# Kernel optimization log

Measured on AMD Instinct MI355X. Metric: run time of the kernel, lower is better.

## Reference

```python
import jax, jax.numpy as jnp
import numpy as np

B, T, RSS, L, FEAT, H = 256, 256, 12, 256, 8, 128
DIST_EPS = 1e-8
LN_EPS = 1e-5

def _lin(x, W, b):
    return x @ W.T + b

def setup_inputs() -> dict:
    key = jax.random.key(0)
    ks = jax.random.split(key, 20)
    w = lambda k, shape: jax.random.normal(k, shape, jnp.float32) * 0.1
    z = lambda *s: jnp.zeros(s, jnp.float32)
    # LED table: xyz positions in a room, frequency index in 1..12 (matches rss channels)
    pos = jax.random.uniform(ks[0], (L, 3), jnp.float32, 0.0, 5.0)
    freq = jax.random.randint(ks[1], (L,), 1, RSS + 1).astype(jnp.float32)
    return dict(
        rss_seq=jax.random.uniform(ks[2], (B, T, RSS), jnp.float32),
        global_led_pos_freq=jnp.concatenate([pos, freq[:, None]], axis=1),
        enc_W1=w(ks[3], (32, 4)), enc_b1=z(32), enc_W2=w(ks[4], (FEAT, 32)), enc_b2=z(FEAT),
        q_W1=w(ks[5], (64, 4)), q_b1=z(64), q_W2=w(ks[6], (64, 64)), q_b2=z(64),
        k_W1=w(ks[7], (64, FEAT + 3)), k_b1=z(64), k_W2=w(ks[8], (64, 64)), k_b2=z(64),
        Wih0=w(ks[9], (4 * H, RSS * (1 + FEAT))), Whh0=w(ks[10], (4 * H, H)), bih0=z(4 * H), bhh0=z(4 * H),
        Wih1=w(ks[11], (4 * H, H)), Whh1=w(ks[12], (4 * H, H)), bih1=z(4 * H), bhh1=z(4 * H),
        ln_g=jnp.ones((H,), jnp.float32), ln_b=z(H),
        fc_W1=w(ks[13], (H // 2, H)), fc_b1=z(H // 2), fc_W2=w(ks[14], (3, H // 2)), fc_b2=z(3),
    )

def _lstm_cell(x, h, c, Wih, Whh, bih, bhh):
    g = x @ Wih.T + bih + h @ Whh.T + bhh  # [B, 4H], pytorch gate order i,f,g,o
    i, f, gg, o = jnp.split(g, 4, axis=-1)
    c = jax.nn.sigmoid(f) * c + jax.nn.sigmoid(i) * jnp.tanh(gg)
    h = jax.nn.sigmoid(o) * jnp.tanh(c)
    return h, c

def _forward(rss_seq, global_led_pos_freq, enc_W1, enc_b1, enc_W2, enc_b2,
             q_W1, q_b1, q_W2, q_b2, k_W1, k_b1, k_W2, k_b2,
             Wih0, Whh0, bih0, bhh0, Wih1, Whh1, bih1, bhh1,
             ln_g, ln_b, fc_W1, fc_b1, fc_W2, fc_b2):
    batch, t_len, rss_dim = rss_seq.shape
    led_pos = global_led_pos_freq[:, :3]   # [L,3]
    led_freq = global_led_pos_freq[:, 3]   # [L]
    rss_freqs = jnp.arange(1, rss_dim + 1, dtype=rss_seq.dtype)
    freq_mask = rss_freqs[:, None] == led_freq[None, :]  # [RSS, L] bool
    # global LED features are a buffer computed under no_grad in torch
    led_feat = jax.lax.stop_gradient(
        jax.nn.relu(_lin(jax.nn.relu(_lin(global_led_pos_freq, enc_W1, enc_b1)), enc_W2, enc_b2)))  # [L,FEAT]
    keys = _lin(jax.nn.relu(_lin(jnp.concatenate([led_feat, led_pos], axis=1), k_W1, k_b1)), k_W2, k_b2)  # [L,64]
    neg = jnp.finfo(rss_seq.dtype).min

    def step(carry, rss_t):
        prev_pos, h0, c0, h1, c1 = carry  # prev_pos [B,3]
        q_in = jnp.concatenate(
            [rss_t[..., None], jnp.broadcast_to(prev_pos[:, None, :], (batch, rss_dim, 3))], axis=-1)  # [B,RSS,4]
        q = _lin(jax.nn.relu(_lin(q_in, q_W1, q_b1)), q_W2, q_b2)  # [B,RSS,64]
        scores = jnp.einsum('bqd,ld->bql', q, keys)  # [B,RSS,L]
        dist_sq = jnp.sum((prev_pos[:, None, :] - led_pos[None, :, :]) ** 2, axis=-1)  # [B,L]
        scores = scores + (-0.5 * jnp.log(dist_sq + DIST_EPS))[:, None, :]
        scores = jnp.where(freq_mask[None], scores, neg)
        attn = jax.nn.softmax(scores, axis=-1)
        agg = jnp.einsum('bql,lf->bqf', attn, led_feat)  # [B,RSS,FEAT]
        x = jnp.concatenate([rss_t[..., None], agg], axis=-1).reshape(batch, -1)  # [B, RSS*(1+FEAT)]
        h0n, c0n = _lstm_cell(x, h0, c0, Wih0, Whh0, bih0, bhh0)
        h1n, c1n = _lstm_cell(h0n, h1, c1, Wih1, Whh1, bih1, bhh1)
        y = h1n
        mu = jnp.mean(y, axis=-1, keepdims=True)
        var = jnp.var(y, axis=-1, keepdims=True)
        y = (y - mu) / jnp.sqrt(var + LN_EPS) * ln_g + ln_b
        pred = _lin(jax.nn.relu(_lin(y, fc_W1, fc_b1)), fc_W2, fc_b2)  # [B,3]
        return (pred, h0n, c0n, h1n, c1n), pred

    prev0 = jnp.broadcast_to(jnp.mean(led_pos, axis=0, keepdims=True), (batch, 3))
    hz = jnp.zeros((batch, Whh0.shape[1]), rss_seq.dtype)
    _, outs = jax.lax.scan(step, (prev0, hz, hz, hz, hz), jnp.swapaxes(rss_seq, 0, 1))
    return jnp.swapaxes(outs, 0, 1)  # [B,T,3]

def reference(rss_seq, global_led_pos_freq, enc_W1, enc_b1, enc_W2, enc_b2,
              q_W1, q_b1, q_W2, q_b2, k_W1, k_b1, k_W2, k_b2,
              Wih0, Whh0, bih0, bhh0, Wih1, Whh1, bih1, bhh1,
              ln_g, ln_b, fc_W1, fc_b1, fc_W2, fc_b2):
    return _forward(rss_seq, global_led_pos_freq, enc_W1, enc_b1, enc_W2, enc_b2,
                    q_W1, q_b1, q_W2, q_b2, k_W1, k_b1, k_W2, k_b2,
                    Wih0, Whh0, bih0, bhh0, Wih1, Whh1, bih1, bhh1,
                    ln_g, ln_b, fc_W1, fc_b1, fc_W2, fc_b2)
```

## Files before the change

kernel.cpp:

```cpp
#include <hip/hip_runtime.h>
#include <hip/hip_fp16.h>
#include <math.h>

#define B_ 256
#define T_ 256
#define RSS_ 12
#define L_ 256
#define FEAT_ 8
#define H_ 128

constexpr int OFF_PW0  = 0;
constexpr int OFF_PW1  = OFF_PW0 + 63488;
constexpr int OFF_W1L  = OFF_PW1 + 32768;
constexpr int OFF_B0   = OFF_W1L + 32768;
constexpr int OFF_B1   = OFF_B0 + 512;
constexpr int OFF_QW1T = OFF_B1 + 512;
constexpr int OFF_FC1  = OFF_QW1T + 256;
constexpr int OFF_K2T4 = OFF_FC1 + 8192;
constexpr int OFF_KB   = OFF_K2T4 + 16384;
constexpr int OFF_LF   = OFF_KB + 256;
constexpr int OFF_LPX  = OFF_LF + 2048;
constexpr int OFF_LPY  = OFF_LPX + 256;
constexpr int OFF_LPZ  = OFF_LPY + 256;
constexpr int OFF_MEAN = OFF_LPZ + 256;
constexpr int OFF_PREV0= OFF_MEAN + 8;
constexpr int OFF_INT  = OFF_PREV0 + 4;

__device__ __forceinline__ unsigned packh2(float a, float b) {
  const unsigned short lo = __half_as_ushort(__float2half(a));
  const unsigned short hi = __half_as_ushort(__float2half(b));
  return (unsigned)lo | ((unsigned)hi << 16);
}
__device__ __forceinline__ __half2 u2h2(unsigned u){ union { unsigned u; __half2 h; } c; c.u = u; return c.h; }
__device__ __forceinline__ float sigf(float x){ return 1.f/(1.f+expf(-x)); }

#if __has_builtin(__builtin_amdgcn_fdot2)
typedef _Float16 h2v __attribute__((ext_vector_type(2)));
__device__ __forceinline__ float d2(unsigned w, unsigned z, float acc) {
  union { unsigned u; h2v h; } cw, cz; cw.u = w; cz.u = z;
  return __builtin_amdgcn_fdot2(cw.h, cz.h, acc, false);
}
#else
__device__ __forceinline__ float d2(unsigned w, unsigned z, float acc) {
  const __half2 hw = u2h2(w), hz = u2h2(z);
  acc = fmaf(__low2float(hw),  __low2float(hz),  acc);
  return fmaf(__high2float(hw), __high2float(hz), acc);
}
#endif

constexpr int SZ_PW0 = 63488, SZ_PW1 = 32768, SZ_W1L = 32768, SZ_B = 512, SZ_Q = 256, SZ_FC = 8192;
constexpr int TOT_T = SZ_PW0 + SZ_PW1 + SZ_W1L + SZ_B + SZ_B + SZ_Q + SZ_FC;

__global__ void k_prep(const float* __restrict__ Wih0, const float* __restrict__ Whh0,
                       const float* __restrict__ bih0, const float* __restrict__ bhh0,
                       const float* __restrict__ Wih1, const float* __restrict__ Whh1,
                       const float* __restrict__ bih1, const float* __restrict__ bhh1,
                       const float* __restrict__ qW1,  const float* __restrict__ fcW1,
                       float* __restrict__ ws) {
  unsigned* wsu = (unsigned*)ws;
  for (int t = blockIdx.x*blockDim.x + threadIdx.x; t < TOT_T; t += gridDim.x*blockDim.x) {
    int u = t;
    if (u < SZ_PW0) {
      const int k = u & 3, j = (u >> 2) & 511, q = u >> 11;
      const int p = 4*q + k;
      float lo, hi;
      if (p < 60) {
        const int r = p / 5, e0 = 2*(p % 5), e1 = e0 + 1;
        lo = Wih0[j*108 + r*9 + e0];
        hi = (e1 <= 8) ? Wih0[j*108 + r*9 + e1] : 0.f;
      } else {
        const int i0 = 2*(p - 60);
        lo = Whh0[j*128 + i0]; hi = Whh0[j*128 + i0 + 1];
      }
      wsu[OFF_PW0 + u] = packh2(lo, hi); continue;
    } u -= SZ_PW0;
    if (u < SZ_PW1) {
      const int k = u & 3, j = (u >> 2) & 511, q = u >> 11;
      const int i0 = 2*(4*q + k);
      wsu[OFF_PW1 + u] = packh2(Wih1[j*128 + i0], Wih1[j*128 + i0 + 1]); continue;
    } u -= SZ_PW1;
    if (u < SZ_W1L) {
      const int k = u & 3, j = (u >> 2) & 511, q = u >> 11;
      const int i0 = 2*(4*q + k);
      wsu[OFF_W1L + u] = packh2(Whh1[j*128 + i0], Whh1[j*128 + i0 + 1]); continue;
    } u -= SZ_W1L;
    if (u < SZ_B) { ws[OFF_B0+u] = bih0[u]+bhh0[u]; continue; } u -= SZ_B;
    if (u < SZ_B) { ws[OFF_B1+u] = bih1[u]+bhh1[u]; continue; } u -= SZ_B;
    if (u < SZ_Q) { const int c=u>>6, j=u&63; ws[OFF_QW1T+u] = qW1[j*4+c]; continue; } u -= SZ_Q;
    { const int c = u >> 8, rem = u & 255, j = rem >> 2, k = rem & 3;
      ws[OFF_FC1 + u] = fcW1[j*128 + (c<<2) + k]; }
  }
}

__global__ __launch_bounds__(256) void k_led(const float* __restrict__ gplf,
    const float* __restrict__ encW1, const float* __restrict__ encb1,
    const float* __restrict__ encW2, const float* __restrict__ encb2,
    const float* __restrict__ kW1, const float* __restrict__ kb1,
    const float* __restrict__ kW2, const float* __restrict__ kb2,
    const float* __restrict__ qW2, const float* __restrict__ qb2,
    float* __restrict__ ws) {
  __shared__ float sLF[L_][FEAT_];
  __shared__ float sP[L_][3];
  __shared__ int   sR[L_];
  const int l = threadIdx.x;
  const float p0=gplf[l*4+0], p1=gplf[l*4+1], p2=gplf[l*4+2], fr=gplf[l*4+3];

  float e1[32];
  for (int j=0;j<32;++j) {
    float v = encb1[j] + encW1[j*4+0]*p0 + encW1[j*4+1]*p1 + encW1[j*4+2]*p2 + encW1[j*4+3]*fr;
    e1[j] = fmaxf(v,0.f);
  }
  float lf[8];
  for (int f=0;f<8;++f) {
    float v = encb2[f];
    for (int j=0;j<32;++j) v += encW2[f*32+j]*e1[j];
    lf[f] = fmaxf(v,0.f);
  }
  float kin[11] = {lf[0],lf[1],lf[2],lf[3],lf[4],lf[5],lf[6],lf[7],p0,p1,p2};
  float hh[64];
  for (int j=0;j<64;++j) {
    float v = kb1[j];
    for (int c=0;c<11;++c) v += kW1[j*11+c]*kin[c];
    hh[j]=fmaxf(v,0.f);
  }
  float kk[64];
  for (int d=0;d<64;++d) {
    float v = kb2[d];
    for (int j=0;j<64;++j) v += kW2[d*64+j]*hh[j];
    kk[d]=v;
  }
  float kbv=0.f;
  for (int d=0;d<64;++d) kbv += qb2[d]*kk[d];
  ws[OFF_KB+l]=kbv;
  for (int e=0;e<64;++e) {
    float acc=0.f;
    for (int d=0;d<64;++d) acc += qW2[d*64+e]*kk[d];
    ws[OFF_K2T4 + (e>>2)*1024 + l*4 + (e&3)] = acc;
  }
  for (int f=0;f<8;++f){ ws[OFF_LF+l*8+f]=lf[f]; sLF[l][f]=lf[f]; }
  ws[OFF_LPX+l]=p0; ws[OFF_LPY+l]=p1; ws[OFF_LPZ+l]=p2;
  sP[l][0]=p0; sP[l][1]=p1; sP[l][2]=p2;
  const int r = (int)fr - 1;
  sR[l]=r;
  int* iws = (int*)(ws + OFF_INT);
  iws[l] = r;
  __syncthreads();
  if (l==0) {
    int* cntp = iws + 256;
    int* idxp = cntp + 16;
    int c[12]; for (int r2=0;r2<12;++r2) c[r2]=0;
    for (int i=0;i<L_;++i){ int r2=sR[i]; idxp[r2*256 + c[r2]] = i; c[r2]++; }
    for (int r2=0;r2<12;++r2) cntp[r2]=c[r2];
    float mx=0.f,my=0.f,mz=0.f;
    for (int i=0;i<L_;++i){mx+=sP[i][0];my+=sP[i][1];mz+=sP[i][2];}
    ws[OFF_PREV0+0]=mx/(float)L_; ws[OFF_PREV0+1]=my/(float)L_; ws[OFF_PREV0+2]=mz/(float)L_;
    for (int f=0;f<8;++f){ float s=0.f; for (int i=0;i<L_;++i) s+=sLF[i][f]; ws[OFF_MEAN+f]=s/(float)L_; }
  }
}

__global__ __launch_bounds__(512,1) void k_main(const float* __restrict__ rss,
    const float* __restrict__ qb1, const float* __restrict__ lng, const float* __restrict__ lnb,
    const float* __restrict__ fcb1, const float* __restrict__ fcW2, const float* __restrict__ fcb2,
    const float* __restrict__ ws, float* __restrict__ out) {
  const int b = blockIdx.x, tid = threadIdx.x;
  const int lane = tid & 63, wave = tid >> 6;
  const int j = tid;

  __shared__ uint4 sW1L[8192];
  __shared__ unsigned sLFh[1024];
  __shared__ float sLPx[256], sLPy[256], sLPz[256];
  __shared__ float sKB[256];
  __shared__ float sQ[256], sqb1v[64];
  __shared__ float sLNG[128], sLNB[128];
  __shared__ float sfcb1[64], sfcW2v[192], sfcb2v[4];
  __shared__ float sMEANv[8];
  __shared__ __align__(16) unsigned sz0h[124];
  __shared__ __align__(16) unsigned sz1h[128];
  __shared__ float sc0[128], sc1[128];
  __shared__ __align__(16) float sa[12][68];
  __shared__ float ssv[256];
  __shared__ float sg[512];
  __shared__ __align__(16) float syv[128];
  __shared__ float sprev[4];
  __shared__ int   sledR[256], scnt[16];
  __shared__ unsigned short sidx16[12*256];

  const uint4* PW0 = (const uint4*)((const unsigned*)ws + OFF_PW0);
  const uint4* PW1 = (const uint4*)((const unsigned*)ws + OFF_PW1);
#define LW0(Q) uint4 w0_##Q = PW0[Q*512 + j];
#define LW1(Q) uint4 w1_##Q = PW1[Q*512 + j];
  LW0(0) LW0(1) LW0(2) LW0(3) LW0(4) LW0(5) LW0(6) LW0(7) LW0(8) LW0(9)
  LW0(10) LW0(11) LW0(12) LW0(13) LW0(14) LW0(15) LW0(16) LW0(17) LW0(18) LW0(19)
  LW0(20) LW0(21) LW0(22) LW0(23) LW0(24) LW0(25) LW0(26) LW0(27) LW0(28) LW0(29) LW0(30)
  LW1(0) LW1(1) LW1(2) LW1(3) LW1(4) LW1(5) LW1(6) LW1(7)
  LW1(8) LW1(9) LW1(10) LW1(11) LW1(12) LW1(13) LW1(14) LW1(15)
  float biasA = ws[OFF_B0 + j];
  float biasB = ws[OFF_B1 + j];
#define PIN4(V) asm volatile("" : "+v"(V.x), "+v"(V.y), "+v"(V.z), "+v"(V.w));
  PIN4(w0_0) PIN4(w0_1) PIN4(w0_2) PIN4(w0_3) PIN4(w0_4) PIN4(w0_5) PIN4(w0_6) PIN4(w0_7)
  PIN4(w0_8) PIN4(w0_9) PIN4(w0_10) PIN4(w0_11) PIN4(w0_12) PIN4(w0_13) PIN4(w0_14) PIN4(w0_15)
  PIN4(w0_16) PIN4(w0_17) PIN4(w0_18) PIN4(w0_19) PIN4(w0_20) PIN4(w0_21) PIN4(w0_22) PIN4(w0_23)
  PIN4(w0_24) PIN4(w0_25) PIN4(w0_26) PIN4(w0_27) PIN4(w0_28) PIN4(w0_29) PIN4(w0_30)
  PIN4(w1_0) PIN4(w1_1) PIN4(w1_2) PIN4(w1_3) PIN4(w1_4) PIN4(w1_5) PIN4(w1_6) PIN4(w1_7)
  PIN4(w1_8) PIN4(w1_9) PIN4(w1_10) PIN4(w1_11) PIN4(w1_12) PIN4(w1_13) PIN4(w1_14) PIN4(w1_15)
  asm volatile("" : "+v"(biasA), "+v"(biasB));

  {
    const uint4* W1Lg = (const uint4*)((const unsigned*)ws + OFF_W1L);
    for (int u = tid; u < 8192; u += 512) sW1L[u] = W1Lg[u];
    for (int u = tid; u < 1024; u += 512) sLFh[u] = packh2(ws[OFF_LF+2*u], ws[OFF_LF+2*u+1]);
  }
  if (tid < 256) { sLPx[tid]=ws[OFF_LPX+tid]; sLPy[tid]=ws[OFF_LPY+tid]; sLPz[tid]=ws[OFF_LPZ+tid];
                   sKB[tid]=ws[OFF_KB+tid]; sQ[tid]=ws[OFF_QW1T+tid]; }
  if (tid < 64) { sqb1v[tid]=qb1[tid]; sfcb1[tid]=fcb1[tid]; }
  if (tid < 128){ sLNG[tid]=lng[tid]; sLNB[tid]=lnb[tid]; sc0[tid]=0.f; sc1[tid]=0.f; sz1h[tid]=0u; }
  if (tid < 192) sfcW2v[tid]=fcW2[tid];
  if (tid < 3)  { sfcb2v[tid]=fcb2[tid]; sprev[tid]=ws[OFF_PREV0+tid]; }
  if (tid < 8)   sMEANv[tid]=ws[OFF_MEAN+tid];
  if (tid < 64)  sz0h[60+tid]=0u;
  {
    const int* iws = (const int*)(ws + OFF_INT);
    if (tid < 256) sledR[tid]=iws[tid];
    if (tid < 12)  scnt[tid]=iws[256+tid];
    for (int u = tid; u < 12*256; u += 512) sidx16[u] = (unsigned short)iws[272+u];
  }
  __syncthreads();

  const float* rb = rss + (size_t)b*T_*12;
  float x0 = rb[wave];
  float x1 = (wave < 4) ? rb[wave+8] : 0.f;

  const float4* K2g = (const float4*)(ws + OFF_K2T4);
  const float4* F1g = (const float4*)(ws + OFF_FC1);
  const uint4*  z0u4 = (const uint4*)sz0h;
  const uint4*  z1u4 = (const uint4*)sz1h;

  for (int t = 0; t < T_; ++t) {
    float xn0 = 0.f, xn1 = 0.f;
    if (t+1 < T_) {
      xn0 = rb[(t+1)*12 + wave];
      if (wave < 4) xn1 = rb[(t+1)*12 + wave+8];
    }
    const float px = sprev[0], py = sprev[1], pz = sprev[2];

    {
      float v = sqb1v[lane] + x0*sQ[lane] + px*sQ[64+lane] + py*sQ[128+lane] + pz*sQ[192+lane];
      sa[wave][lane] = fmaxf(v, 0.f);
      if (wave < 4) {
        float v2 = sqb1v[lane] + x1*sQ[lane] + px*sQ[64+lane] + py*sQ[128+lane] + pz*sQ[192+lane];
        sa[wave+8][lane] = fmaxf(v2, 0.f);
      }
    }
    __syncthreads();

    if (tid < 256) {
      const int l = tid, r = sledR[l];
      float a0 = sKB[l], a1 = 0.f;
      const float4* ar4 = (const float4*)&sa[r][0];
      #pragma unroll 1
      for (int cc = 0; cc < 4; ++cc) {
        const float4 wA = K2g[(cc*4+0)*256 + l];
        const float4 wB = K2g[(cc*4+1)*256 + l];
        const float4 wC = K2g[(cc*4+2)*256 + l];
        const float4 wD = K2g[(cc*4+3)*256 + l];
        const float4 aA = ar4[cc*4+0], aB = ar4[cc*4+1], aC = ar4[cc*4+2], aD = ar4[cc*4+3];
        a0=fmaf(aA.x,wA.x,a0); a1=fmaf(aA.y,wA.y,a1); a0=fmaf(aA.z,wA.z,a0); a1=fmaf(aA.w,wA.w,a1);
        a0=fmaf(aB.x,wB.x,a0); a1=fmaf(aB.y,wB.y,a1); a0=fmaf(aB.z,wB.z,a0); a1=fmaf(aB.w,wB.w,a1);
        a0=fmaf(aC.x,wC.x,a0); a1=fmaf(aC.y,wC.y,a1); a0=fmaf(aC.z,wC.z,a0); a1=fmaf(aC.w,wC.w,a1);
        a0=fmaf(aD.x,wD.x,a0); a1=fmaf(aD.y,wD.y,a1); a0=fmaf(aD.z,wD.z,a0); a1=fmaf(aD.w,wD.w,a1);
      }
      const float dx = px-sLPx[tid], dy = py-sLPy[tid], dz = pz-sLPz[tid];
      ssv[tid] = a0 + a1 - 0.5f*logf(dx*dx+dy*dy+dz*dz + 1e-8f);
    }
    __syncthreads();

    for (int rr = 0; rr < 2; ++rr) {
      if (rr == 1 && wave >= 4) break;
      const int r = wave + rr*8;
      const int cnt = scnt[r];
      float vmax = -3.402823466e38f;
      for (int c = lane; c < cnt; c += 64) vmax = fmaxf(vmax, ssv[sidx16[r*256+c]]);
      #pragma unroll
      for (int o = 32; o > 0; o >>= 1) vmax = fmaxf(vmax, __shfl_xor(vmax, o));
      float ps=0.f, p0=0.f,p1=0.f,p2=0.f,p3=0.f,p4=0.f,p5=0.f,p6=0.f,p7=0.f;
      for (int c = lane; c < cnt; c += 64) {
        const int li = sidx16[r*256+c];
        const float p = expf(ssv[li]-vmax);
        ps += p;
        const unsigned* lf = sLFh + li*4;
        const __half2 A=u2h2(lf[0]), Bq=u2h2(lf[1]), C=u2h2(lf[2]), D=u2h2(lf[3]);
        p0 += p*__low2float(A); p1 += p*__high2float(A);
        p2 += p*__low2float(Bq); p3 += p*__high2float(Bq);
        p4 += p*__low2float(C); p5 += p*__high2float(C);
        p6 += p*__low2float(D); p7 += p*__high2float(D);
      }
      #pragma unroll
      for (int o = 32; o > 0; o >>= 1) {
        ps += __shfl_xor(ps,o);
        p0 += __shfl_xor(p0,o); p1 += __shfl_xor(p1,o);
        p2 += __shfl_xor(p2,o); p3 += __shfl_xor(p3,o);
        p4 += __shfl_xor(p4,o); p5 += __shfl_xor(p5,o);
        p6 += __shfl_xor(p6,o); p7 += __shfl_xor(p7,o);
      }
      if (lane == 0) {
        const float xv = rr ? x1 : x0;
        float a0v,a1v,a2v,a3v,a4v,a5v,a6v,a7v;
        if (cnt > 0) {
          const float inv = 1.f/ps;
          a0v=p0*inv; a1v=p1*inv; a2v=p2*inv; a3v=p3*inv;
          a4v=p4*inv; a5v=p5*inv; a6v=p6*inv; a7v=p7*inv;
        } else {
          a0v=sMEANv[0]; a1v=sMEANv[1]; a2v=sMEANv[2]; a3v=sMEANv[3];
          a4v=sMEANv[4]; a5v=sMEANv[5]; a6v=sMEANv[6]; a7v=sMEANv[7];
        }
        sz0h[r*5+0] = packh2(xv,  a0v);
        sz0h[r*5+1] = packh2(a1v, a2v);
        sz0h[r*5+2] = packh2(a3v, a4v);
        sz0h[r*5+3] = packh2(a5v, a6v);
        sz0h[r*5+4] = packh2(a7v, 0.f);
      }
    }
    __syncthreads();

    {
      float g0 = biasA, g1 = 0.f, g2 = 0.f, g3 = 0.f;
#define D0(Q) { const uint4 Z = z0u4[Q]; \
      g0 = d2(w0_##Q.x, Z.x, g0); g1 = d2(w0_##Q.y, Z.y, g1); \
      g2 = d2(w0_##Q.z, Z.z, g2); g3 = d2(w0_##Q.w, Z.w, g3); }
      D0(0) D0(1) D0(2) D0(3) D0(4) D0(5) D0(6) D0(7) D0(8) D0(9)
      D0(10) D0(11) D0(12) D0(13) D0(14) D0(15) D0(16) D0(17) D0(18) D0(19)
      D0(20) D0(21) D0(22) D0(23) D0(24) D0(25) D0(26) D0(27) D0(28) D0(29) D0(30)
      sg[j] = (g0+g1)+(g2+g3);
    }
    __syncthreads();

    if (tid < 64) {
      const int v = tid;
      const float iA=sigf(sg[2*v]),     iB=sigf(sg[2*v+1]);
      const float fA=sigf(sg[128+2*v]), fB=sigf(sg[128+2*v+1]);
      const float gA=tanhf(sg[256+2*v]),gB=tanhf(sg[256+2*v+1]);
      const float oA=sigf(sg[384+2*v]), oB=sigf(sg[384+2*v+1]);
      const float cA = fA*sc0[2*v]   + iA*gA;
      const float cB = fB*sc0[2*v+1] + iB*gB;
      sc0[2*v] = cA; sc0[2*v+1] = cB;
      const float hA = oA*tanhf(cA), hB = oB*tanhf(cB);
      const unsigned hp = packh2(hA, hB);
      sz0h[60+v] = hp; sz1h[v] = hp;
    }
    __syncthreads();

    {
      float g0 = biasB, g1 = 0.f, g2 = 0.f, g3 = 0.f;
#define E1(Q) { const uint4 Z = z1u4[Q]; \
      g0 = d2(w1_##Q.x, Z.x, g0); g1 = d2(w1_##Q.y, Z.y, g1); \
      g2 = d2(w1_##Q.z, Z.z, g2); g3 = d2(w1_##Q.w, Z.w, g3); }
      E1(0) E1(1) E1(2) E1(3) E1(4) E1(5) E1(6) E1(7)
      E1(8) E1(9) E1(10) E1(11) E1(12) E1(13) E1(14) E1(15)
      #pragma unroll 4
      for (int q = 0; q < 16; ++q) {
        const uint4 W = sW1L[q*512 + j];
        const uint4 Z = z1u4[16+q];
        g0 = d2(W.x, Z.x, g0); g1 = d2(W.y, Z.y, g1);
        g2 = d2(W.z, Z.z, g2); g3 = d2(W.w, Z.w, g3);
      }
      sg[j] = (g0+g1)+(g2+g3);
    }
    __syncthreads();

    if (tid < 64) {
      const int v = tid;
      const float iA=sigf(sg[2*v]),     iB=sigf(sg[2*v+1]);
      const float fA=sigf(sg[128+2*v]), fB=sigf(sg[128+2*v+1]);
      const float gA=tanhf(sg[256+2*v]),gB=tanhf(sg[256+2*v+1]);
      const float oA=sigf(sg[384+2*v]), oB=sigf(sg[384+2*v+1]);
      const float cA = fA*sc1[2*v]   + iA*gA;
      const float cB = fB*sc1[2*v+1] + iB*gB;
      sc1[2*v] = cA; sc1[2*v+1] = cB;
      const float hA = oA*tanhf(cA), hB = oB*tanhf(cB);
      sz1h[64+v] = packh2(hA, hB);
      float s = hA + hB, qs = hA*hA + hB*hB;
      #pragma unroll
      for (int o = 32; o > 0; o >>= 1) { s += __shfl_xor(s,o); qs += __shfl_xor(qs,o); }
      const float mu = s*(1.f/128.f);
      const float rs = 1.f/sqrtf(qs*(1.f/128.f) - mu*mu + 1e-5f);
      const float yA = (hA-mu)*rs*sLNG[2*v] + sLNB[2*v];
      const float yB = (hB-mu)*rs*sLNG[2*v+1] + sLNB[2*v+1];
      syv[2*v] = yA; syv[2*v+1] = yB;
      float acc = sfcb1[v], acc2 = 0.f;
      const float4* sy4 = (const float4*)syv;
      #pragma unroll 1
      for (int cc = 0; cc < 8; ++cc) {
        const float4 wA = F1g[(cc*4+0)*64 + v];
        const float4 wB = F1g[(cc*4+1)*64 + v];
        const float4 wC = F1g[(cc*4+2)*64 + v];
        const float4 wD = F1g[(cc*4+3)*64 + v];
        const float4 zA = sy4[cc*4+0], zB = sy4[cc*4+1], zC = sy4[cc*4+2], zD = sy4[cc*4+3];
        acc=fmaf(wA.x,zA.x,acc); acc2=fmaf(wA.y,zA.y,acc2); acc=fmaf(wA.z,zA.z,acc); acc2=fmaf(wA.w,zA.w,acc2);
        acc=fmaf(wB.x,zB.x,acc); acc2=fmaf(wB.y,zB.y,acc2); acc=fmaf(wB.z,zB.z,acc); acc2=fmaf(wB.w,zB.w,acc2);
        acc=fmaf(wC.x,zC.x,acc); acc2=fmaf(wC.y,zC.y,acc2); acc=fmaf(wC.z,zC.z,acc); acc2=fmaf(wC.w,zC.w,acc2);
        acc=fmaf(wD.x,zD.x,acc); acc2=fmaf(wD.y,zD.y,acc2); acc=fmaf(wD.z,zD.z,acc); acc2=fmaf(wD.w,zD.w,acc2);
      }
      const float f1 = fmaxf(acc+acc2, 0.f);
      float a0 = sfcW2v[v]*f1, a1 = sfcW2v[64+v]*f1, a2 = sfcW2v[128+v]*f1;
      #pragma unroll
      for (int o = 32; o > 0; o >>= 1) {
        a0 += __shfl_xor(a0,o); a1 += __shfl_xor(a1,o); a2 += __shfl_xor(a2,o);
      }
      if (v < 3) {
        const float r = (v==0 ? a0 : (v==1 ? a1 : a2)) + sfcb2v[v];
        out[((size_t)b*T_+t)*3+v] = r;
        sprev[v] = r;
      }
    }
    __syncthreads();

    x0 = xn0; x1 = xn1;
  }
}

extern "C" void kernel_launch(void* const* d_in, const int* in_sizes, int n_in,
                              void* d_out, int out_size, void* d_ws, size_t ws_size,
                              hipStream_t stream) {
  const float* rss   = (const float*)d_in[0];
  const float* gplf  = (const float*)d_in[1];
  const float* encW1 = (const float*)d_in[2];
  const float* encb1 = (const float*)d_in[3];
  const float* encW2 = (const float*)d_in[4];
  const float* encb2 = (const float*)d_in[5];
  const float* qW1   = (const float*)d_in[6];
  const float* qb1   = (const float*)d_in[7];
  const float* qW2   = (const float*)d_in[8];
  const float* qb2   = (const float*)d_in[9];
  const float* kW1   = (const float*)d_in[10];
  const float* kb1   = (const float*)d_in[11];
  const float* kW2   = (const float*)d_in[12];
  const float* kb2   = (const float*)d_in[13];
  const float* Wih0  = (const float*)d_in[14];
  const float* Whh0  = (const float*)d_in[15];
  const float* bih0  = (const float*)d_in[16];
  const float* bhh0  = (const float*)d_in[17];
  const float* Wih1  = (const float*)d_in[18];
  const float* Whh1  = (const float*)d_in[19];
  const float* bih1  = (const float*)d_in[20];
  const float* bhh1  = (const float*)d_in[21];
  const float* lng   = (const float*)d_in[22];
  const float* lnb   = (const float*)d_in[23];
  const float* fcW1  = (const float*)d_in[24];
  const float* fcb1  = (const float*)d_in[25];
  const float* fcW2  = (const float*)d_in[26];
  const float* fcb2  = (const float*)d_in[27];
  float* ws   = (float*)d_ws;
  float* outp = (float*)d_out;

  hipLaunchKernelGGL(k_prep, dim3(256), dim3(256), 0, stream,
                     Wih0,Whh0,bih0,bhh0,Wih1,Whh1,bih1,bhh1,qW1,fcW1,ws);
  hipLaunchKernelGGL(k_led, dim3(1), dim3(256), 0, stream,
                     gplf,encW1,encb1,encW2,encb2,kW1,kb1,kW2,kb2,qW2,qb2,ws);
  hipLaunchKernelGGL(k_main, dim3(B_), dim3(512), 0, stream,
                     rss,qb1,lng,lnb,fcb1,fcW2,fcb2,ws,outp);
}
```

Baseline: 2.746 ms.

## Double block to 1024 threads, split LSTM gate dot products across halves

Launches k_main with 1024 threads per block. Each LSTM gate row's reduction over the packed input/hidden vector is split between two thread halves, and the partial sums are combined through a two-slot shared buffer before the activations. The LED key MLP is spread over four threads per LED with a shuffle reduction, and each frequency channel gets its own wave. The aim is to shorten the serial per-timestep critical path and halve the register-pinned weights per thread, at the cost of more synchronising threads and an extra shared-memory add per gate.

```diff
diff --git a/kernel.cpp b/kernel.cpp
--- a/kernel.cpp
+++ b/kernel.cpp
@@ -158,13 +158,13 @@
   }
 }
 
-__global__ __launch_bounds__(512,1) void k_main(const float* __restrict__ rss,
+__global__ __launch_bounds__(1024) void k_main(const float* __restrict__ rss,
     const float* __restrict__ qb1, const float* __restrict__ lng, const float* __restrict__ lnb,
     const float* __restrict__ fcb1, const float* __restrict__ fcW2, const float* __restrict__ fcb2,
     const float* __restrict__ ws, float* __restrict__ out) {
   const int b = blockIdx.x, tid = threadIdx.x;
   const int lane = tid & 63, wave = tid >> 6;
-  const int j = tid;
+  const int j = tid & 511, h = tid >> 9;
 
   __shared__ uint4 sW1L[8192];
   __shared__ unsigned sLFh[1024];
@@ -179,7 +179,7 @@
   __shared__ float sc0[128], sc1[128];
   __shared__ __align__(16) float sa[12][68];
   __shared__ float ssv[256];
-  __shared__ float sg[512];
+  __shared__ float sgp[2][512];
   __shared__ __align__(16) float syv[128];
   __shared__ float sprev[4];
   __shared__ int   sledR[256], scnt[16];
@@ -187,48 +187,45 @@
 
   const uint4* PW0 = (const uint4*)((const unsigned*)ws + OFF_PW0);
   const uint4* PW1 = (const uint4*)((const unsigned*)ws + OFF_PW1);
-#define LW0(Q) uint4 w0_##Q = PW0[Q*512 + j];
-#define LW1(Q) uint4 w1_##Q = PW1[Q*512 + j];
-  LW0(0) LW0(1) LW0(2) LW0(3) LW0(4) LW0(5) LW0(6) LW0(7) LW0(8) LW0(9)
-  LW0(10) LW0(11) LW0(12) LW0(13) LW0(14) LW0(15) LW0(16) LW0(17) LW0(18) LW0(19)
-  LW0(20) LW0(21) LW0(22) LW0(23) LW0(24) LW0(25) LW0(26) LW0(27) LW0(28) LW0(29) LW0(30)
+  const int zb0 = h * 15;
+#define LW0(Q) uint4 w0_##Q = PW0[(zb0+Q)*512 + j];
+  LW0(0) LW0(1) LW0(2) LW0(3) LW0(4) LW0(5) LW0(6) LW0(7)
+  LW0(8) LW0(9) LW0(10) LW0(11) LW0(12) LW0(13) LW0(14)
+  uint4 w0x = h ? PW0[30*512 + j] : make_uint4(0,0,0,0);
+#define LW1(Q) uint4 w1_##Q = PW1[(h*8+Q)*512 + j];
   LW1(0) LW1(1) LW1(2) LW1(3) LW1(4) LW1(5) LW1(6) LW1(7)
-  LW1(8) LW1(9) LW1(10) LW1(11) LW1(12) LW1(13) LW1(14) LW1(15)
-  float biasA = ws[OFF_B0 + j];
-  float biasB = ws[OFF_B1 + j];
+  float biasA = h ? 0.f : ws[OFF_B0 + j];
+  float biasB = h ? 0.f : ws[OFF_B1 + j];
 #define PIN4(V) asm volatile("" : "+v"(V.x), "+v"(V.y), "+v"(V.z), "+v"(V.w));
   PIN4(w0_0) PIN4(w0_1) PIN4(w0_2) PIN4(w0_3) PIN4(w0_4) PIN4(w0_5) PIN4(w0_6) PIN4(w0_7)
-  PIN4(w0_8) PIN4(w0_9) PIN4(w0_10) PIN4(w0_11) PIN4(w0_12) PIN4(w0_13) PIN4(w0_14) PIN4(w0_15)
-  PIN4(w0_16) PIN4(w0_17) PIN4(w0_18) PIN4(w0_19) PIN4(w0_20) PIN4(w0_21) PIN4(w0_22) PIN4(w0_23)
-  PIN4(w0_24) PIN4(w0_25) PIN4(w0_26) PIN4(w0_27) PIN4(w0_28) PIN4(w0_29) PIN4(w0_30)
+  PIN4(w0_8) PIN4(w0_9) PIN4(w0_10) PIN4(w0_11) PIN4(w0_12) PIN4(w0_13) PIN4(w0_14) PIN4(w0x)
   PIN4(w1_0) PIN4(w1_1) PIN4(w1_2) PIN4(w1_3) PIN4(w1_4) PIN4(w1_5) PIN4(w1_6) PIN4(w1_7)
-  PIN4(w1_8) PIN4(w1_9) PIN4(w1_10) PIN4(w1_11) PIN4(w1_12) PIN4(w1_13) PIN4(w1_14) PIN4(w1_15)
   asm volatile("" : "+v"(biasA), "+v"(biasB));
 
   {
     const uint4* W1Lg = (const uint4*)((const unsigned*)ws + OFF_W1L);
-    for (int u = tid; u < 8192; u += 512) sW1L[u] = W1Lg[u];
-    for (int u = tid; u < 1024; u += 512) sLFh[u] = packh2(ws[OFF_LF+2*u], ws[OFF_LF+2*u+1]);
+    for (int u = tid; u < 8192; u += 1024) sW1L[u] = W1Lg[u];
+    for (int u = tid; u < 1024; u += 1024) sLFh[u] = packh2(ws[OFF_LF+2*u], ws[OFF_LF+2*u+1]);
   }
   if (tid < 256) { sLPx[tid]=ws[OFF_LPX+tid]; sLPy[tid]=ws[OFF_LPY+tid]; sLPz[tid]=ws[OFF_LPZ+tid];
                    sKB[tid]=ws[OFF_KB+tid]; sQ[tid]=ws[OFF_QW1T+tid]; }
-  if (tid < 64) { sqb1v[tid]=qb1[tid]; sfcb1[tid]=fcb1[tid]; }
-  if (tid < 128){ sLNG[tid]=lng[tid]; sLNB[tid]=lnb[tid]; sc0[tid]=0.f; sc1[tid]=0.f; sz1h[tid]=0u; }
-  if (tid < 192) sfcW2v[tid]=fcW2[tid];
-  if (tid < 3)  { sfcb2v[tid]=fcb2[tid]; sprev[tid]=ws[OFF_PREV0+tid]; }
-  if (tid < 8)   sMEANv[tid]=ws[OFF_MEAN+tid];
-  if (tid < 64)  sz0h[60+tid]=0u;
+  else if (tid >= 256 && tid < 320) { sqb1v[tid-256]=qb1[tid-256]; sfcb1[tid-256]=fcb1[tid-256]; }
+  else if (tid >= 320 && tid < 448) { sLNG[tid-320]=lng[tid-320]; sLNB[tid-320]=lnb[tid-320];
+                                      sc0[tid-320]=0.f; sc1[tid-320]=0.f; sz1h[tid-320]=0u; }
+  else if (tid >= 448 && tid < 640) sfcW2v[tid-448]=fcW2[tid-448];
+  else if (tid >= 640 && tid < 643) { sfcb2v[tid-640]=fcb2[tid-640]; sprev[tid-640]=ws[OFF_PREV0+tid-640]; }
+  else if (tid >= 648 && tid < 656) sMEANv[tid-648]=ws[OFF_MEAN+tid-648];
+  else if (tid >= 656 && tid < 720) sz0h[60+(tid-656)]=0u;
   {
     const int* iws = (const int*)(ws + OFF_INT);
-    if (tid < 256) sledR[tid]=iws[tid];
-    if (tid < 12)  scnt[tid]=iws[256+tid];
-    for (int u = tid; u < 12*256; u += 512) sidx16[u] = (unsigned short)iws[272+u];
+    if (tid >= 720 && tid < 976) sledR[tid-720]=iws[tid-720];
+    if (tid >= 976 && tid < 988) scnt[tid-976]=iws[256+(tid-976)];
+    for (int u = tid; u < 12*256; u += 1024) sidx16[u] = (unsigned short)iws[272+u];
   }
   __syncthreads();
 
   const float* rb = rss + (size_t)b*T_*12;
-  float x0 = rb[wave];
-  float x1 = (wave < 4) ? rb[wave+8] : 0.f;
+  float x0 = (wave < 12) ? rb[wave] : 0.f;
 
   const float4* K2g = (const float4*)(ws + OFF_K2T4);
   const float4* F1g = (const float4*)(ws + OFF_FC1);
@@ -236,48 +233,41 @@
   const uint4*  z1u4 = (const uint4*)sz1h;
 
   for (int t = 0; t < T_; ++t) {
-    float xn0 = 0.f, xn1 = 0.f;
-    if (t+1 < T_) {
-      xn0 = rb[(t+1)*12 + wave];
-      if (wave < 4) xn1 = rb[(t+1)*12 + wave+8];
-    }
+    float xn0 = 0.f;
+    if (t+1 < T_ && wave < 12) xn0 = rb[(t+1)*12 + wave];
     const float px = sprev[0], py = sprev[1], pz = sprev[2];
 
-    {
+    if (tid < 768) {
       float v = sqb1v[lane] + x0*sQ[lane] + px*sQ[64+lane] + py*sQ[128+lane] + pz*sQ[192+lane];
       sa[wave][lane] = fmaxf(v, 0.f);
-      if (wave < 4) {
-        float v2 = sqb1v[lane] + x1*sQ[lane] + px*sQ[64+lane] + py*sQ[128+lane] + pz*sQ[192+lane];
-        sa[wave+8][lane] = fmaxf(v2, 0.f);
-      }
-    }
-    __syncthreads();
-
-    if (tid < 256) {
-      const int l = tid, r = sledR[l];
-      float a0 = sKB[l], a1 = 0.f;
+    }
+    __syncthreads();
+
+    {
+      const int l = tid >> 2, k = tid & 3;
+      const int r = sledR[l];
       const float4* ar4 = (const float4*)&sa[r][0];
-      #pragma unroll 1
-      for (int cc = 0; cc < 4; ++cc) {
-        const float4 wA = K2g[(cc*4+0)*256 + l];
-        const float4 wB = K2g[(cc*4+1)*256 + l];
-        const float4 wC = K2g[(cc*4+2)*256 + l];
-        const float4 wD = K2g[(cc*4+3)*256 + l];
-        const float4 aA = ar4[cc*4+0], aB = ar4[cc*4+1], aC = ar4[cc*4+2], aD = ar4[cc*4+3];
-        a0=fmaf(aA.x,wA.x,a0); a1=fmaf(aA.y,wA.y,a1); a0=fmaf(aA.z,wA.z,a0); a1=fmaf(aA.w,wA.w,a1);
-        a0=fmaf(aB.x,wB.x,a0); a1=fmaf(aB.y,wB.y,a1); a0=fmaf(aB.z,wB.z,a0); a1=fmaf(aB.w,wB.w,a1);
-        a0=fmaf(aC.x,wC.x,a0); a1=fmaf(aC.y,wC.y,a1); a0=fmaf(aC.z,wC.z,a0); a1=fmaf(aC.w,wC.w,a1);
-        a0=fmaf(aD.x,wD.x,a0); a1=fmaf(aD.y,wD.y,a1); a0=fmaf(aD.z,wD.z,a0); a1=fmaf(aD.w,wD.w,a1);
-      }
-      const float dx = px-sLPx[tid], dy = py-sLPy[tid], dz = pz-sLPz[tid];
-      ssv[tid] = a0 + a1 - 0.5f*logf(dx*dx+dy*dy+dz*dz + 1e-8f);
-    }
-    __syncthreads();
-
-    for (int rr = 0; rr < 2; ++rr) {
-      if (rr == 1 && wave >= 4) break;
-      const int r = wave + rr*8;
-      const int cnt = scnt[r];
+      float a0 = 0.f, a1 = 0.f;
+      #pragma unroll
+      for (int c2 = 0; c2 < 4; ++c2) {
+        const int cc = k*4 + c2;
+        const float4 w = K2g[cc*256 + l];
+        const float4 a = ar4[cc];
+        a0 = fmaf(a.x, w.x, a0); a1 = fmaf(a.y, w.y, a1);
+        a0 = fmaf(a.z, w.z, a0); a1 = fmaf(a.w, w.w, a1);
+      }
+      float s = a0 + a1;
+      s += __shfl_xor(s, 1);
+      s += __shfl_xor(s, 2);
+      if (k == 0) {
+        const float dx = px-sLPx[l], dy = py-sLPy[l], dz = pz-sLPz[l];
+        ssv[l] = s + sKB[l] - 0.5f*logf(dx*dx+dy*dy+dz*dz + 1e-8f);
+      }
+    }
+    __syncthreads();
+
+    if (wave < 12) {
+      const int r = wave, cnt = scnt[r];
       float vmax = -3.402823466e38f;
       for (int c = lane; c < cnt; c += 64) vmax = fmaxf(vmax, ssv[sidx16[r*256+c]]);
       #pragma unroll
@@ -303,7 +293,6 @@
         p6 += __shfl_xor(p6,o); p7 += __shfl_xor(p7,o);
       }
       if (lane == 0) {
-        const float xv = rr ? x1 : x0;
         float a0v,a1v,a2v,a3v,a4v,a5v,a6v,a7v;
         if (cnt > 0) {
           const float inv = 1.f/ps;
@@ -313,7 +302,7 @@
           a0v=sMEANv[0]; a1v=sMEANv[1]; a2v=sMEANv[2]; a3v=sMEANv[3];
           a4v=sMEANv[4]; a5v=sMEANv[5]; a6v=sMEANv[6]; a7v=sMEANv[7];
         }
-        sz0h[r*5+0] = packh2(xv,  a0v);
+        sz0h[r*5+0] = packh2(x0,  a0v);
         sz0h[r*5+1] = packh2(a1v, a2v);
         sz0h[r*5+2] = packh2(a3v, a4v);
         sz0h[r*5+3] = packh2(a5v, a6v);
@@ -324,26 +313,30 @@
 
     {
       float g0 = biasA, g1 = 0.f, g2 = 0.f, g3 = 0.f;
-#define D0(Q) { const uint4 Z = z0u4[Q]; \
+#define D0(Q) { const uint4 Z = z0u4[zb0+Q]; \
       g0 = d2(w0_##Q.x, Z.x, g0); g1 = d2(w0_##Q.y, Z.y, g1); \
       g2 = d2(w0_##Q.z, Z.z, g2); g3 = d2(w0_##Q.w, Z.w, g3); }
-      D0(0) D0(1) D0(2) D0(3) D0(4) D0(5) D0(6) D0(7) D0(8) D0(9)
-      D0(10) D0(11) D0(12) D0(13) D0(14) D0(15) D0(16) D0(17) D0(18) D0(19)
-      D0(20) D0(21) D0(22) D0(23) D0(24) D0(25) D0(26) D0(27) D0(28) D0(29) D0(30)
-      sg[j] = (g0+g1)+(g2+g3);
+      D0(0) D0(1) D0(2) D0(3) D0(4) D0(5) D0(6) D0(7)
+      D0(8) D0(9) D0(10) D0(11) D0(12) D0(13) D0(14)
+      if (h) {
+        const uint4 Z = z0u4[30];
+        g0 = d2(w0x.x, Z.x, g0); g1 = d2(w0x.y, Z.y, g1);
+        g2 = d2(w0x.z, Z.z, g2); g3 = d2(w0x.w, Z.w, g3);
+      }
+      sgp[h][j] = (g0+g1)+(g2+g3);
     }
     __syncthreads();
 
     if (tid < 64) {
       const int v = tid;
-      const float iA=sigf(sg[2*v]),     iB=sigf(sg[2*v+1]);
-      const float fA=sigf(sg[128+2*v]), fB=sigf(sg[128+2*v+1]);
-      const float gA=tanhf(sg[256+2*v]),gB=tanhf(sg[256+2*v+1]);
-      const float oA=sigf(sg[384+2*v]), oB=sigf(sg[384+2*v+1]);
-      const float cA = fA*sc0[2*v]   + iA*gA;
-      const float cB = fB*sc0[2*v+1] + iB*gB;
+      const float giA = sgp[0][2*v]+sgp[1][2*v],     giB = sgp[0][2*v+1]+sgp[1][2*v+1];
+      const float gfA = sgp[0][128+2*v]+sgp[1][128+2*v], gfB = sgp[0][129+2*v]+sgp[1][129+2*v];
+      const float ggA = sgp[0][256+2*v]+sgp[1][256+2*v], ggB = sgp[0][257+2*v]+sgp[1][257+2*v];
+      const float goA = sgp[0][384+2*v]+sgp[1][384+2*v], goB = sgp[0][385+2*v]+sgp[1][385+2*v];
+      const float cA = sigf(gfA)*sc0[2*v]   + sigf(giA)*tanhf(ggA);
+      const float cB = sigf(gfB)*sc0[2*v+1] + sigf(giB)*tanhf(ggB);
       sc0[2*v] = cA; sc0[2*v+1] = cB;
-      const float hA = oA*tanhf(cA), hB = oB*tanhf(cB);
+      const float hA = sigf(goA)*tanhf(cA), hB = sigf(goB)*tanhf(cB);
       const unsigned hp = packh2(hA, hB);
       sz0h[60+v] = hp; sz1h[v] = hp;
     }
@@ -351,32 +344,32 @@
 
     {
       float g0 = biasB, g1 = 0.f, g2 = 0.f, g3 = 0.f;
-#define E1(Q) { const uint4 Z = z1u4[Q]; \
+      const int zb1 = h*8;
+#define E1(Q) { const uint4 Z = z1u4[zb1+Q]; \
       g0 = d2(w1_##Q.x, Z.x, g0); g1 = d2(w1_##Q.y, Z.y, g1); \
       g2 = d2(w1_##Q.z, Z.z, g2); g3 = d2(w1_##Q.w, Z.w, g3); }
       E1(0) E1(1) E1(2) E1(3) E1(4) E1(5) E1(6) E1(7)
-      E1(8) E1(9) E1(10) E1(11) E1(12) E1(13) E1(14) E1(15)
-      #pragma unroll 4
-      for (int q = 0; q < 16; ++q) {
-        const uint4 W = sW1L[q*512 + j];
-        const uint4 Z = z1u4[16+q];
+      #pragma unroll
+      for (int q = 0; q < 8; ++q) {
+        const uint4 W = sW1L[(zb1+q)*512 + j];
+        const uint4 Z = z1u4[16+zb1+q];
         g0 = d2(W.x, Z.x, g0); g1 = d2(W.y, Z.y, g1);
         g2 = d2(W.z, Z.z, g2); g3 = d2(W.w, Z.w, g3);
       }
-      sg[j] = (g0+g1)+(g2+g3);
+      sgp[h][j] = (g0+g1)+(g2+g3);
     }
     __syncthreads();
 
     if (tid < 64) {
       const int v = tid;
-      const float iA=sigf(sg[2*v]),     iB=sigf(sg[2*v+1]);
-      const float fA=sigf(sg[128+2*v]), fB=sigf(sg[128+2*v+1]);
-      const float gA=tanhf(sg[256+2*v]),gB=tanhf(sg[256+2*v+1]);
-      const float oA=sigf(sg[384+2*v]), oB=sigf(sg[384+2*v+1]);
-      const float cA = fA*sc1[2*v]   + iA*gA;
-      const float cB = fB*sc1[2*v+1] + iB*gB;
+      const float giA = sgp[0][2*v]+sgp[1][2*v],     giB = sgp[0][2*v+1]+sgp[1][2*v+1];
+      const float gfA = sgp[0][128+2*v]+sgp[1][128+2*v], gfB = sgp[0][129+2*v]+sgp[1][129+2*v];
+      const float ggA = sgp[0][256+2*v]+sgp[1][256+2*v], ggB = sgp[0][257+2*v]+sgp[1][257+2*v];
+      const float goA = sgp[0][384+2*v]+sgp[1][384+2*v], goB = sgp[0][385+2*v]+sgp[1][385+2*v];
+      const float cA = sigf(gfA)*sc1[2*v]   + sigf(giA)*tanhf(ggA);
+      const float cB = sigf(gfB)*sc1[2*v+1] + sigf(giB)*tanhf(ggB);
       sc1[2*v] = cA; sc1[2*v+1] = cB;
-      const float hA = oA*tanhf(cA), hB = oB*tanhf(cB);
+      const float hA = sigf(goA)*tanhf(cA), hB = sigf(goB)*tanhf(cB);
       sz1h[64+v] = packh2(hA, hB);
       float s = hA + hB, qs = hA*hA + hB*hB;
       #pragma unroll
@@ -414,7 +407,7 @@
     }
     __syncthreads();
 
-    x0 = xn0; x1 = xn1;
+    x0 = xn0;
   }
 }
 
@@ -456,6 +449,6 @@
                      Wih0,Whh0,bih0,bhh0,Wih1,Whh1,bih1,bhh1,qW1,fcW1,ws);
   hipLaunchKernelGGL(k_led, dim3(1), dim3(256), 0, stream,
                      gplf,encW1,encb1,encW2,encb2,kW1,kb1,kW2,kb2,qW2,qb2,ws);
-  hipLaunchKernelGGL(k_main, dim3(B_), dim3(512), 0, stream,
+  hipLaunchKernelGGL(k_main, dim3(B_), dim3(1024), 0, stream,
                      rss,qb1,lng,lnb,fcb1,fcW2,fcb2,ws,outp);
 }
```

Result: slower. 7.702 ms (+180.5%).
